# Kernel optimization log

Hardware: AMD Instinct MI355X
Metric: run time of the kernel (lower is better)

## Reference

```python
import jax, jax.numpy as jnp
import numpy as np

B, N, IN_DIM, D, H, E, L = 4, 1024, 128, 512, 8, 4, 3
HD = D // H
LN_EPS = 1e-5


def setup_inputs() -> dict:
    key = jax.random.key(0)
    ks = jax.random.split(key, 16)
    s = lambda fan_in: 1.0 / np.sqrt(fan_in)
    inp = {
        'x': jax.random.normal(ks[0], (B, N, IN_DIM), dtype=jnp.float32),
        'edges': jax.random.normal(ks[1], (B, N, N, E), dtype=jnp.float32),
        'in_w': jax.random.normal(ks[2], (IN_DIM, D), dtype=jnp.float32) * s(IN_DIM),
        'in_b': jnp.zeros((D,), dtype=jnp.float32),
        'qw': jax.random.normal(ks[3], (L, D, D), dtype=jnp.float32) * s(D),
        'qb': jnp.zeros((L, D), dtype=jnp.float32),
        'kw': jax.random.normal(ks[4], (L, D, D), dtype=jnp.float32) * s(D),
        'kb': jnp.zeros((L, D), dtype=jnp.float32),
        'vw': jax.random.normal(ks[5], (L, D, D), dtype=jnp.float32) * s(D),
        'vb': jnp.zeros((L, D), dtype=jnp.float32),
        'ow': jax.random.normal(ks[6], (L, D, D), dtype=jnp.float32) * s(D),
        'ob': jnp.zeros((L, D), dtype=jnp.float32),
        'ew': jax.random.normal(ks[7], (L, E, H), dtype=jnp.float32) * s(E),
        'eb': jnp.zeros((L, H), dtype=jnp.float32),
        'ln_g': jnp.ones((D,), dtype=jnp.float32),
        'ln_b': jnp.zeros((D,), dtype=jnp.float32),
    }
    return inp


def _gat_layer(h, edges, qw, qb, kw, kb, vw, vb, ow, ob, ew, eb):
    # h: (B, N, D); edges: (B, N, N, E)
    q = (h @ qw + qb).reshape(B, N, H, HD)
    k = (h @ kw + kb).reshape(B, N, H, HD)
    v = (h @ vw + vb).reshape(B, N, H, HD)
    logits = jnp.einsum('bihd,bjhd->bhij', q, k) / np.sqrt(HD).astype(np.float32)
    bias = jnp.einsum('bije,eh->bhij', edges, ew) + eb[None, :, None, None]
    attn = jax.nn.softmax(logits + bias, axis=-1)  # (B, H, N, N)
    out = jnp.einsum('bhij,bjhd->bihd', attn, v).reshape(B, N, D)
    return out @ ow + ob


def reference(x, edges, in_w, in_b, qw, qb, kw, kb, vw, vb, ow, ob, ew, eb, ln_g, ln_b):
    h = x @ in_w + in_b  # (B, N, D)
    for l in range(L):
        h = h + _gat_layer(h, edges, qw[l], qb[l], kw[l], kb[l], vw[l], vb[l],
                           ow[l], ob[l], ew[l], eb[l])
    mu = jnp.mean(h, axis=-1, keepdims=True)
    var = jnp.mean(jnp.square(h - mu), axis=-1, keepdims=True)
    return (h - mu) * jax.lax.rsqrt(var + LN_EPS) * ln_g + ln_b
```

## Files before the change

kernel.cpp:

```cpp
#include <hip/hip_runtime.h>
#include <hip/hip_bf16.h>
#include <cstdint>
#include <cstddef>

#define BB 4
#define NN 1024
#define INDIM 128
#define DD 512
#define HH 8
#define EE 4
#define LL 3
#define HDIM 64

typedef __bf16 bf16x8 __attribute__((ext_vector_type(8)));
typedef _Float16 f16x8 __attribute__((ext_vector_type(8)));
typedef _Float16 h2 __attribute__((ext_vector_type(2)));
typedef float f32x4 __attribute__((ext_vector_type(4)));
typedef unsigned int u32x4 __attribute__((ext_vector_type(4)));

__device__ __forceinline__ unsigned short f2b(float f) {
    union { float f; unsigned int u; } v; v.f = f;
    unsigned int u = v.u;
    unsigned int r = (u + 0x7FFFu + ((u >> 16) & 1u)) >> 16;
    return (unsigned short)r;
}
__device__ __forceinline__ float b2f(unsigned int us) {
    union { unsigned int u; float f; } v; v.u = us << 16; return v.f;
}
__device__ __forceinline__ unsigned short h_bits(_Float16 h) {
    union { _Float16 h; unsigned short u; } v; v.h = h; return v.u;
}
__device__ __forceinline__ h2 u2h2(unsigned int u) {
    union { unsigned int u; h2 h; } v; v.u = u; return v.h;
}
__device__ __forceinline__ unsigned int pkrtz_u32(float a, float b) {
    auto h = __builtin_amdgcn_cvt_pkrtz(a, b);
    union { decltype(h) h; unsigned int u; } v; v.h = h; return v.u;
}

__device__ __forceinline__ void gl_lds16(const unsigned short* g, unsigned short* l) {
    __builtin_amdgcn_global_load_lds(
        (const __attribute__((address_space(1))) void*)g,
        (__attribute__((address_space(3))) void*)l, 16, 0, 0);
}

__device__ __forceinline__ void transpose_tile_body(const float* __restrict__ src,
                                                    unsigned short* __restrict__ dst,
                                                    int K, int Nc) {
    __shared__ float tl[32][33];
    const int n0 = blockIdx.x * 32, k0 = blockIdx.y * 32;
    const int tx = threadIdx.x, ty = threadIdx.y;
#pragma unroll
    for (int r = 0; r < 4; r++) {
        int k = ty + r * 8;
        tl[k][tx] = src[(size_t)(k0 + k) * Nc + n0 + tx];
    }
    __syncthreads();
#pragma unroll
    for (int r = 0; r < 4; r++) {
        int n = ty + r * 8;
        dst[(size_t)(n0 + n) * K + k0 + tx] = f2b(tl[tx][n]);
    }
}

__global__ void k_transpose_in(const float* __restrict__ w, unsigned short* __restrict__ dst) {
    transpose_tile_body(w, dst, INDIM, DD);
}

__global__ void k_transpose_qkvo(const float* __restrict__ qw, const float* __restrict__ kw,
                                 const float* __restrict__ vw, const float* __restrict__ ow,
                                 unsigned short* __restrict__ dst) {
    int zz = blockIdx.z;
    int l = zz >> 2, tsel = zz & 3;
    const float* src = (tsel == 0) ? qw : (tsel == 1) ? kw : (tsel == 2) ? vw : ow;
    src += (size_t)l * DD * DD;
    transpose_tile_body(src, dst + (size_t)zz * DD * DD, DD, DD);
}

__global__ void k_convert(const float* __restrict__ src, unsigned short* __restrict__ dst,
                          long long n4) {
    long long stride = (long long)gridDim.x * blockDim.x;
    for (long long i = blockIdx.x * (long long)blockDim.x + threadIdx.x; i < n4; i += stride) {
        float4 v = reinterpret_cast<const float4*>(src)[i];
        uint2 o;
        o.x = (unsigned)f2b(v.x) | ((unsigned)f2b(v.y) << 16);
        o.y = (unsigned)f2b(v.z) | ((unsigned)f2b(v.w) << 16);
        reinterpret_cast<uint2*>(dst)[i] = o;
    }
}

__global__ __launch_bounds__(256) void k_convert_e2(const float* __restrict__ src,
                                                    unsigned short* __restrict__ dst) {
    __shared__ unsigned short tl[4096];
    const int tile = blockIdx.x;
    const int jb = tile & 15;
    const int it = (tile >> 4) & 63;
    const int b  = tile >> 10;
    const int tid = threadIdx.x;
    const int f4 = tid & 63;
    const int r0 = tid >> 6;
    const int jt = f4 >> 4, w16 = f4 & 15;
    const int lh = w16 >> 2, rr = w16 & 3;
    const int c = jt * 2 + (rr >> 1), q = rr & 1;
#pragma unroll
    for (int rd = 0; rd < 4; rd++) {
        const int lm = rd * 4 + r0;
        const float4 e = *reinterpret_cast<const float4*>(
            &src[(((size_t)b * NN + it * 16 + lm) * NN + jb * 64 + f4) * EE]);
        uint2 o;
        o.x = pkrtz_u32(e.x, e.y);
        o.y = pkrtz_u32(e.z, e.w);
        const int slot = c * 128 + (lh * 16 + lm) * 2 + q;
        *reinterpret_cast<uint2*>(&tl[slot * 4]) = o;
    }
    __syncthreads();
    u32x4* g = reinterpret_cast<u32x4*>(dst) + (size_t)tile * 512;
    const u32x4* s = reinterpret_cast<const u32x4*>(tl);
    __builtin_nontemporal_store(s[tid], g + tid);
    __builtin_nontemporal_store(s[tid + 256], g + tid + 256);
}

__global__ __launch_bounds__(256) void k_gemm(
    const unsigned short* __restrict__ A,
    const unsigned short* __restrict__ Wt0, size_t wstride,
    const float* __restrict__ bias0, const float* __restrict__ bias1, const float* __restrict__ bias2,
    unsigned short* __restrict__ outb, size_t ostride,
    unsigned short* __restrict__ vt_out,
    const unsigned short* __restrict__ residb,
    int Kd)
{
    __shared__ __align__(16) unsigned short As[128 * 32];
    __shared__ __align__(16) unsigned short Bs[64 * 32];
    const int tid = threadIdx.x;
    const int lane = tid & 63, wv = tid >> 6;
    const int wr = wv >> 1, wc = wv & 1;
    const int lm = lane & 15, lh = lane >> 4;
    const int m0 = blockIdx.y * 128, n0 = blockIdx.x * 64;
    const int z = blockIdx.z;
    const unsigned short* Wt = Wt0 + (size_t)z * wstride;
    const float* bias = (z == 0) ? bias0 : (z == 1) ? bias1 : bias2;

    f32x4 acc[4][2] = {};

    const int o0 = tid * 16;
    const int rowA = o0 >> 6, colA = (o0 & 63) >> 1;
    for (int k0 = 0; k0 < Kd; k0 += 32) {
        __syncthreads();
        gl_lds16(A  + (size_t)(m0 + rowA) * Kd + k0 + colA, As + (o0 >> 1));
        gl_lds16(A  + (size_t)(m0 + 64 + rowA) * Kd + k0 + colA, As + 2048 + (o0 >> 1));
        gl_lds16(Wt + (size_t)(n0 + rowA) * Kd + k0 + colA, Bs + (o0 >> 1));
        __syncthreads();

        bf16x8 af[4], bfg[2];
#pragma unroll
        for (int mi = 0; mi < 4; mi++)
            af[mi] = *reinterpret_cast<const bf16x8*>(&As[(wr * 64 + mi * 16 + lm) * 32 + lh * 8]);
#pragma unroll
        for (int nj = 0; nj < 2; nj++)
            bfg[nj] = *reinterpret_cast<const bf16x8*>(&Bs[(wc * 32 + nj * 16 + lm) * 32 + lh * 8]);
        __builtin_amdgcn_s_setprio(1);
#pragma unroll
        for (int mi = 0; mi < 4; mi++)
#pragma unroll
            for (int nj = 0; nj < 2; nj++)
                acc[mi][nj] = __builtin_amdgcn_mfma_f32_16x16x32_bf16(af[mi], bfg[nj], acc[mi][nj], 0, 0, 0);
        __builtin_amdgcn_s_setprio(0);
    }

    if (vt_out && z == 2) {
        const int j = n0 + wc * 32 + lm;
#pragma unroll
        for (int mi = 0; mi < 4; mi++) {
            const int i = m0 + wr * 64 + mi * 16 + lh * 4;
            const int bb = i >> 10, n = i & (NN - 1);
#pragma unroll
            for (int nj = 0; nj < 2; nj++) {
                const int jj = j + nj * 16;
                const int hh = jj >> 6, d = jj & 63;
                union { unsigned short us[4]; uint2 u; } pk;
#pragma unroll
                for (int r = 0; r < 4; r++)
                    pk.us[r] = h_bits((_Float16)(acc[mi][nj][r] + bias[jj]));
                *reinterpret_cast<uint2*>(
                    &vt_out[(((size_t)bb * HH + hh) * HDIM + d) * NN + n]) = pk.u;
            }
        }
        return;
    }

#pragma unroll
    for (int mi = 0; mi < 4; mi++) {
#pragma unroll
        for (int nj = 0; nj < 2; nj++) {
#pragma unroll
            for (int r = 0; r < 4; r++) {
                int i = m0 + wr * 64 + mi * 16 + lh * 4 + r;
                int j = n0 + wc * 32 + nj * 16 + lm;
                float val = acc[mi][nj][r] + bias[j];
                size_t oidx = (size_t)i * DD + j;
                if (residb) val += b2f(residb[oidx]);
                outb[(size_t)z * ostride + oidx] = f2b(val);
            }
        }
    }
}

template <int JS>
__global__ __launch_bounds__(512) void k_attn_g2(
    const unsigned short* __restrict__ qb,
    const unsigned short* __restrict__ kb,
    const unsigned short* __restrict__ vt,
    const unsigned short* __restrict__ ebt,
    const float* __restrict__ ew,
    const float* __restrict__ ebias,
    int layer,
    unsigned short* __restrict__ outpb,
    float2* __restrict__ mlp)
{
    __shared__ __align__(16) unsigned short e_lds[2][2][4096];
    __shared__ unsigned short p_lds[8][2][16 * 68];
    const int lin = blockIdx.x;
    const int xcd = lin & 7;
    const int s   = lin >> 3;
    const int combo = xcd * 2 + (s >> 5);
    const int itg = s & 31;
    const int b  = combo & 3;
    const int js = combo >> 2;
    const int tid = threadIdx.x;
    const int lane = tid & 63, wv = tid >> 6;
    const int h = wv;
    const int lm = lane & 15, lh = lane >> 4;

    const float LOG2E = 1.44269504f;
    const float ebh = ebias[layer * HH + h] * LOG2E;
    const float qscale = 0.125f * LOG2E;
    h2 w01, w23;
    w01.x = (_Float16)(ew[(layer * EE + 0) * HH + h] * LOG2E);
    w01.y = (_Float16)(ew[(layer * EE + 1) * HH + h] * LOG2E);
    w23.x = (_Float16)(ew[(layer * EE + 2) * HH + h] * LOG2E);
    w23.y = (_Float16)(ew[(layer * EE + 3) * HH + h] * LOG2E);

    bf16x8 aq[2][2];
#pragma unroll
    for (int g = 0; g < 2; g++) {
        const unsigned short* qrow =
            qb + ((size_t)(b * NN) + itg * 32 + g * 16 + lm) * DD + h * HDIM + lh * 8;
        aq[g][0] = *reinterpret_cast<const bf16x8*>(qrow);
        aq[g][1] = *reinterpret_cast<const bf16x8*>(qrow + 32);
    }

    f32x4 acc[2][4] = {};
    float m_run[2] = {-1e30f, -1e30f}, l_run[2] = {0.f, 0.f};

    constexpr int NITER = (NN / JS) / 64;
    const int jlo = js * (NN / JS);
    const int jb0 = jlo >> 6;
    const unsigned short* etile0 = ebt + ((size_t)((b * 64 + itg * 2 + 0) * 16 + jb0)) * 4096;
    const unsigned short* etile1 = ebt + ((size_t)((b * 64 + itg * 2 + 1) * 16 + jb0)) * 4096;
    const unsigned short* kptr = kb + ((size_t)(b * NN) + jlo + lm) * DD + h * HDIM + lh * 8;
    const unsigned short* vptr = vt + (((size_t)(b * HH) + h) * HDIM + lm) * NN + jlo + lh * 8;

    gl_lds16(etile0 + tid * 8, &e_lds[0][0][tid * 8]);
    gl_lds16(etile1 + tid * 8, &e_lds[0][1][tid * 8]);
    __syncthreads();

#pragma unroll
    for (int i = 0; i < NITER; i++) {
        const int cur = i & 1;
        if (i + 1 < NITER) {
            gl_lds16(etile0 + (size_t)(i + 1) * 4096 + tid * 8, &e_lds[cur ^ 1][0][tid * 8]);
            gl_lds16(etile1 + (size_t)(i + 1) * 4096 + tid * 8, &e_lds[cur ^ 1][1][tid * 8]);
        }

        bf16x8 kf[8];
        f16x8  vf[8];
#pragma unroll
        for (int jt = 0; jt < 4; jt++) {
            const unsigned short* kr = kptr + (size_t)i * 64 * DD + (size_t)jt * 16 * DD;
            kf[jt * 2]     = *reinterpret_cast<const bf16x8*>(kr);
            kf[jt * 2 + 1] = *reinterpret_cast<const bf16x8*>(kr + 32);
        }
#pragma unroll
        for (int kc = 0; kc < 2; kc++)
#pragma unroll
            for (int dt = 0; dt < 4; dt++)
                vf[kc * 4 + dt] = *reinterpret_cast<const f16x8*>(
                    vptr + (size_t)dt * 16 * NN + i * 64 + kc * 32);

#pragma unroll
        for (int g = 0; g < 2; g++) {
            f32x4 sreg[4];
#pragma unroll
            for (int jt = 0; jt < 4; jt++) {
                f32x4 t = {};
                t = __builtin_amdgcn_mfma_f32_16x16x32_bf16(kf[jt * 2], aq[g][0], t, 0, 0, 0);
                t = __builtin_amdgcn_mfma_f32_16x16x32_bf16(kf[jt * 2 + 1], aq[g][1], t, 0, 0, 0);
                sreg[jt] = t;
            }

            float pv[16];
#pragma unroll
            for (int c = 0; c < 8; c++) {
                const uint4 ee = *reinterpret_cast<const uint4*>(
                    &e_lds[cur][g][(c * 64 + lane) * 8]);
                const int jt = c >> 1, r0 = (c & 1) * 2;
                pv[jt * 4 + r0] = fmaf(sreg[jt][r0], qscale,
                    __builtin_amdgcn_fdot2(u2h2(ee.x), w01,
                        __builtin_amdgcn_fdot2(u2h2(ee.y), w23, ebh, false), false));
                pv[jt * 4 + r0 + 1] = fmaf(sreg[jt][r0 + 1], qscale,
                    __builtin_amdgcn_fdot2(u2h2(ee.z), w01,
                        __builtin_amdgcn_fdot2(u2h2(ee.w), w23, ebh, false), false));
            }

            float mt = pv[0];
#pragma unroll
            for (int q = 1; q < 16; q++) mt = fmaxf(mt, pv[q]);
            mt = fmaxf(mt, __shfl_xor(mt, 16));
            mt = fmaxf(mt, __shfl_xor(mt, 32));
            float mn = fmaxf(m_run[g], mt);
            float corr = __builtin_amdgcn_exp2f(m_run[g] - mn);
            m_run[g] = mn;
            float ls = 0.f;
#pragma unroll
            for (int q = 0; q < 16; q++) {
                pv[q] = __builtin_amdgcn_exp2f(pv[q] - mn);
                ls += pv[q];
            }
            ls += __shfl_xor(ls, 16);
            ls += __shfl_xor(ls, 32);
            l_run[g] = l_run[g] * corr + ls;

#pragma unroll
            for (int jt = 0; jt < 4; jt++) {
                uint2 u;
                u.x = pkrtz_u32(pv[jt * 4 + 0], pv[jt * 4 + 1]);
                u.y = pkrtz_u32(pv[jt * 4 + 2], pv[jt * 4 + 3]);
                *reinterpret_cast<uint2*>(&p_lds[wv][g][lm * 68 + jt * 16 + lh * 4]) = u;
            }
#pragma unroll
            for (int dt = 0; dt < 4; dt++)
#pragma unroll
                for (int r = 0; r < 4; r++) acc[g][dt][r] *= corr;

#pragma unroll
            for (int kc = 0; kc < 2; kc++) {
                f16x8 pb = *reinterpret_cast<const f16x8*>(
                    &p_lds[wv][g][lm * 68 + kc * 32 + lh * 8]);
#pragma unroll
                for (int dt = 0; dt < 4; dt++)
                    acc[g][dt] = __builtin_amdgcn_mfma_f32_16x16x32_f16(
                        vf[kc * 4 + dt], pb, acc[g][dt], 0, 0, 0);
            }
        }

        __syncthreads();
    }

#pragma unroll
    for (int g = 0; g < 2; g++) {
        const int irow = itg * 32 + g * 16 + lm;
#pragma unroll
        for (int dt = 0; dt < 4; dt++) {
            union { unsigned short us[4]; uint2 u; } pk;
#pragma unroll
            for (int r = 0; r < 4; r++) pk.us[r] = f2b(acc[g][dt][r]);
            *reinterpret_cast<uint2*>(
                &outpb[((size_t)(js * BB + b) * NN + irow) * DD + h * HDIM + dt * 16 + lh * 4]) = pk.u;
        }
        if (lh == 0)
            mlp[((size_t)(js * BB + b) * HH + h) * NN + irow] = make_float2(m_run[g], l_run[g]);
    }
}

template <int JS>
__global__ __launch_bounds__(256) void k_attnred(
    const unsigned short* __restrict__ outpb, const float2* __restrict__ mlp,
    unsigned short* __restrict__ attnob)
{
    const int tid = blockIdx.x * 256 + threadIdx.x;
    const int dc = tid & 7;
    const int h = (tid >> 3) & 7;
    const int n = (tid >> 6) & (NN - 1);
    const int b = tid >> 16;
    float ms[JS], lsv[JS];
    float mstar = -1e30f;
#pragma unroll
    for (int s2 = 0; s2 < JS; s2++) {
        float2 ml = mlp[((size_t)(s2 * BB + b) * HH + h) * NN + n];
        ms[s2] = ml.x; lsv[s2] = ml.y;
        mstar = fmaxf(mstar, ml.x);
    }
    float lstar = 0.f;
    float o[8] = {0.f, 0.f, 0.f, 0.f, 0.f, 0.f, 0.f, 0.f};
#pragma unroll
    for (int s2 = 0; s2 < JS; s2++) {
        float w = __builtin_amdgcn_exp2f(ms[s2] - mstar);
        lstar += w * lsv[s2];
        uint4 a = *reinterpret_cast<const uint4*>(
            &outpb[((size_t)(s2 * BB + b) * NN + n) * DD + h * HDIM + dc * 8]);
        o[0] += w * b2f(a.x & 0xffffu); o[1] += w * b2f(a.x >> 16);
        o[2] += w * b2f(a.y & 0xffffu); o[3] += w * b2f(a.y >> 16);
        o[4] += w * b2f(a.z & 0xffffu); o[5] += w * b2f(a.z >> 16);
        o[6] += w * b2f(a.w & 0xffffu); o[7] += w * b2f(a.w >> 16);
    }
    const float inv = 1.f / lstar;
    union { unsigned short us[8]; uint4 u; } pk;
#pragma unroll
    for (int q = 0; q < 8; q++) pk.us[q] = f2b(o[q] * inv);
    *reinterpret_cast<uint4*>(&attnob[((size_t)b * NN + n) * DD + h * HDIM + dc * 8]) = pk.u;
}

__global__ __launch_bounds__(256) void k_ln(const unsigned short* __restrict__ hb,
                                            const float* __restrict__ g,
                                            const float* __restrict__ bta,
                                            float* __restrict__ out) {
    const int row = blockIdx.x * 4 + (threadIdx.x >> 6);
    const int lane = threadIdx.x & 63;
    const unsigned short* hr = hb + (size_t)row * DD + lane * 8;
    uint4 v = *reinterpret_cast<const uint4*>(hr);
    float vals[8] = { b2f(v.x & 0xffffu), b2f(v.x >> 16), b2f(v.y & 0xffffu), b2f(v.y >> 16),
                      b2f(v.z & 0xffffu), b2f(v.z >> 16), b2f(v.w & 0xffffu), b2f(v.w >> 16) };
    float sum = 0.f, sq = 0.f;
#pragma unroll
    for (int q = 0; q < 8; q++) { sum += vals[q]; sq += vals[q] * vals[q]; }
#pragma unroll
    for (int m = 1; m <= 32; m <<= 1) {
        sum += __shfl_xor(sum, m);
        sq += __shfl_xor(sq, m);
    }
    float mu = sum * (1.f / DD);
    float var = sq * (1.f / DD) - mu * mu;
    float rs = rsqrtf(var + 1e-5f);
    const float* gp = g + lane * 8;
    const float* bp = bta + lane * 8;
    float* op = out + (size_t)row * DD + lane * 8;
#pragma unroll
    for (int q = 0; q < 8; q++) op[q] = (vals[q] - mu) * rs * gp[q] + bp[q];
}

extern "C" void kernel_launch(void* const* d_in, const int* in_sizes, int n_in,
                              void* d_out, int out_size, void* d_ws, size_t ws_size,
                              hipStream_t stream) {
    (void)in_sizes; (void)n_in; (void)out_size; (void)ws_size;
    const float* x     = (const float*)d_in[0];
    const float* edges = (const float*)d_in[1];
    const float* in_w  = (const float*)d_in[2];
    const float* in_b  = (const float*)d_in[3];
    const float* qw    = (const float*)d_in[4];
    const float* qbias = (const float*)d_in[5];
    const float* kw    = (const float*)d_in[6];
    const float* kbias = (const float*)d_in[7];
    const float* vw    = (const float*)d_in[8];
    const float* vbias = (const float*)d_in[9];
    const float* ow    = (const float*)d_in[10];
    const float* obias = (const float*)d_in[11];
    const float* ew    = (const float*)d_in[12];
    const float* ebias = (const float*)d_in[13];
    const float* ln_g  = (const float*)d_in[14];
    const float* ln_b  = (const float*)d_in[15];
    float* out = (float*)d_out;

    constexpr int JS = 4;
    char* ws = (char*)d_ws;
    size_t off = 0;
    auto alloc = [&](size_t bytes) -> void* {
        void* p = ws + off;
        off += (bytes + 255) & ~(size_t)255;
        return p;
    };
    const size_t M = (size_t)BB * NN;
    unsigned short* hb    = (unsigned short*)alloc(M * DD * 2);
    unsigned short* xb    = (unsigned short*)alloc(M * INDIM * 2);
    unsigned short* wt_in = (unsigned short*)alloc((size_t)DD * INDIM * 2);
    unsigned short* wt    = (unsigned short*)alloc((size_t)12 * DD * DD * 2);
    unsigned short* qkvb  = (unsigned short*)alloc((size_t)3 * M * DD * 2);
    unsigned short* vtb   = (unsigned short*)alloc(M * DD * 2);
    unsigned short* attnob= (unsigned short*)alloc(M * DD * 2);
    const size_t edgeElems = (size_t)BB * NN * NN * EE;
    unsigned short* ebt   = (unsigned short*)alloc(edgeElems * 2);
    unsigned short* outpb = (unsigned short*)alloc((size_t)JS * M * DD * 2);
    float2*         mlp   = (float2*)        alloc((size_t)JS * BB * HH * NN * 8);
    const size_t BND = M * DD;

    k_transpose_in<<<dim3(DD / 32, INDIM / 32), dim3(32, 8), 0, stream>>>(in_w, wt_in);
    k_transpose_qkvo<<<dim3(DD / 32, DD / 32, 12), dim3(32, 8), 0, stream>>>(qw, kw, vw, ow, wt);
    k_convert<<<dim3(512), dim3(256), 0, stream>>>(x, xb, (long long)(M * INDIM / 4));
    k_convert_e2<<<dim3(4096), dim3(256), 0, stream>>>(edges, ebt);

    k_gemm<<<dim3(8, 32, 1), dim3(256), 0, stream>>>(
        xb, wt_in, (size_t)0, in_b, in_b, in_b, hb, (size_t)0,
        (unsigned short*)nullptr, (const unsigned short*)nullptr, INDIM);

    for (int l = 0; l < LL; l++) {
        k_gemm<<<dim3(8, 32, 3), dim3(256), 0, stream>>>(
            hb, wt + (size_t)(l * 4) * DD * DD, (size_t)DD * DD,
            qbias + l * DD, kbias + l * DD, vbias + l * DD,
            qkvb, BND, vtb, (const unsigned short*)nullptr, DD);

        k_attn_g2<JS><<<dim3(512), dim3(512), 0, stream>>>(
            qkvb, qkvb + BND, vtb, ebt, ew, ebias, l, outpb, mlp);
        k_attnred<JS><<<dim3((unsigned)(M * HH * 8 / 256)), dim3(256), 0, stream>>>(
            outpb, mlp, attnob);

        k_gemm<<<dim3(8, 32, 1), dim3(256), 0, stream>>>(
            attnob, wt + (size_t)(l * 4 + 3) * DD * DD, (size_t)0,
            obias + l * DD, obias + l * DD, obias + l * DD,
            hb, (size_t)0, (unsigned short*)nullptr, hb, DD);
    }

    k_ln<<<dim3((unsigned)(M / 4)), dim3(256), 0, stream>>>(hb, ln_g, ln_b, out);
}
```

Before: 290.7 us.

## Fuse split-softmax reduction into output projection GEMM prologue

Removes the separate attention-reduction kernel and folds the combination of the JS partial attention outputs, using the running max and sum values, into the A-tile load of the output-projection GEMM. This drops one kernel launch per layer and the write and re-read of the intermediate attention-output buffer. In exchange, each GEMM block now reads JS partial tiles per K step, recomputes the reduction weights for every column block (eight times redundantly), and converts through registers into LDS instead of loading A asynchronously.

Result: slower. 326.0 us (+12.1%).

```diff
diff --git a/kernel.cpp b/kernel.cpp
--- a/kernel.cpp
+++ b/kernel.cpp
@@ -200,6 +200,148 @@
                 size_t oidx = (size_t)i * DD + j;
                 if (residb) val += b2f(residb[oidx]);
                 outb[(size_t)z * ostride + oidx] = f2b(val);
+            }
+        }
+    }
+}
+
+template <int JS>
+__global__ __launch_bounds__(256) void k_gemm_red(
+    const unsigned short* __restrict__ outpb,
+    const float2* __restrict__ mlp,
+    const unsigned short* __restrict__ Wt,
+    const float* __restrict__ bias,
+    unsigned short* __restrict__ outb,
+    const unsigned short* __restrict__ residb)
+{
+    __shared__ __align__(16) unsigned short As[128 * 32];
+    __shared__ __align__(16) unsigned short Bs[64 * 32];
+    const int tid = threadIdx.x;
+    const int lane = tid & 63, wv = tid >> 6;
+    const int wr = wv >> 1, wc = wv & 1;
+    const int lm = lane & 15, lh = lane >> 4;
+    const int m0 = blockIdx.y * 128, n0 = blockIdx.x * 64;
+    const size_t BND = (size_t)BB * NN * DD;
+
+    f32x4 acc[4][2] = {};
+
+    const int o0 = tid * 16;
+    const int rowA = o0 >> 6, colA = (o0 & 63) >> 1;
+    const int i_lo = m0 + rowA, i_hi = m0 + 64 + rowA;
+    const int bidx = m0 >> 10;
+    const int n_lo = i_lo & (NN - 1), n_hi = i_hi & (NN - 1);
+
+#pragma unroll
+    for (int h8 = 0; h8 < 8; h8++) {
+        float w_lo[JS], w_hi[JS];
+        {
+            float msv[JS], lsv[JS], mstar = -1e30f;
+#pragma unroll
+            for (int s = 0; s < JS; s++) {
+                float2 ml = mlp[((size_t)(s * BB + bidx) * HH + h8) * NN + n_lo];
+                msv[s] = ml.x; lsv[s] = ml.y; mstar = fmaxf(mstar, ml.x);
+            }
+            float lstar = 0.f;
+#pragma unroll
+            for (int s = 0; s < JS; s++) {
+                w_lo[s] = __builtin_amdgcn_exp2f(msv[s] - mstar);
+                lstar += w_lo[s] * lsv[s];
+            }
+            const float inv = 1.f / lstar;
+#pragma unroll
+            for (int s = 0; s < JS; s++) w_lo[s] *= inv;
+        }
+        {
+            float msv[JS], lsv[JS], mstar = -1e30f;
+#pragma unroll
+            for (int s = 0; s < JS; s++) {
+                float2 ml = mlp[((size_t)(s * BB + bidx) * HH + h8) * NN + n_hi];
+                msv[s] = ml.x; lsv[s] = ml.y; mstar = fmaxf(mstar, ml.x);
+            }
+            float lstar = 0.f;
+#pragma unroll
+            for (int s = 0; s < JS; s++) {
+                w_hi[s] = __builtin_amdgcn_exp2f(msv[s] - mstar);
+                lstar += w_hi[s] * lsv[s];
+            }
+            const float inv = 1.f / lstar;
+#pragma unroll
+            for (int s = 0; s < JS; s++) w_hi[s] *= inv;
+        }
+
+#pragma unroll
+        for (int kk = 0; kk < 2; kk++) {
+            const int k0 = h8 * 64 + kk * 32;
+
+            uint4 alo[JS], ahi[JS];
+#pragma unroll
+            for (int s = 0; s < JS; s++) {
+                alo[s] = *reinterpret_cast<const uint4*>(
+                    &outpb[(size_t)s * BND + (size_t)i_lo * DD + k0 + colA]);
+                ahi[s] = *reinterpret_cast<const uint4*>(
+                    &outpb[(size_t)s * BND + (size_t)i_hi * DD + k0 + colA]);
+            }
+            union { unsigned short us[8]; uint4 u; } plo, phi;
+            {
+                float o[8] = {0,0,0,0,0,0,0,0};
+#pragma unroll
+                for (int s = 0; s < JS; s++) {
+                    o[0] += w_lo[s] * b2f(alo[s].x & 0xffffu); o[1] += w_lo[s] * b2f(alo[s].x >> 16);
+                    o[2] += w_lo[s] * b2f(alo[s].y & 0xffffu); o[3] += w_lo[s] * b2f(alo[s].y >> 16);
+                    o[4] += w_lo[s] * b2f(alo[s].z & 0xffffu); o[5] += w_lo[s] * b2f(alo[s].z >> 16);
+                    o[6] += w_lo[s] * b2f(alo[s].w & 0xffffu); o[7] += w_lo[s] * b2f(alo[s].w >> 16);
+                }
+#pragma unroll
+                for (int q = 0; q < 8; q++) plo.us[q] = f2b(o[q]);
+            }
+            {
+                float o[8] = {0,0,0,0,0,0,0,0};
+#pragma unroll
+                for (int s = 0; s < JS; s++) {
+                    o[0] += w_hi[s] * b2f(ahi[s].x & 0xffffu); o[1] += w_hi[s] * b2f(ahi[s].x >> 16);
+                    o[2] += w_hi[s] * b2f(ahi[s].y & 0xffffu); o[3] += w_hi[s] * b2f(ahi[s].y >> 16);
+                    o[4] += w_hi[s] * b2f(ahi[s].z & 0xffffu); o[5] += w_hi[s] * b2f(ahi[s].z >> 16);
+                    o[6] += w_hi[s] * b2f(ahi[s].w & 0xffffu); o[7] += w_hi[s] * b2f(ahi[s].w >> 16);
+                }
+#pragma unroll
+                for (int q = 0; q < 8; q++) phi.us[q] = f2b(o[q]);
+            }
+
+            __syncthreads();
+            *reinterpret_cast<uint4*>(&As[o0 >> 1]) = plo.u;
+            *reinterpret_cast<uint4*>(&As[2048 + (o0 >> 1)]) = phi.u;
+            gl_lds16(Wt + (size_t)(n0 + rowA) * DD + k0 + colA, Bs + (o0 >> 1));
+            __syncthreads();
+
+            bf16x8 af[4], bfg[2];
+#pragma unroll
+            for (int mi = 0; mi < 4; mi++)
+                af[mi] = *reinterpret_cast<const bf16x8*>(&As[(wr * 64 + mi * 16 + lm) * 32 + lh * 8]);
+#pragma unroll
+            for (int nj = 0; nj < 2; nj++)
+                bfg[nj] = *reinterpret_cast<const bf16x8*>(&Bs[(wc * 32 + nj * 16 + lm) * 32 + lh * 8]);
+            __builtin_amdgcn_s_setprio(1);
+#pragma unroll
+            for (int mi = 0; mi < 4; mi++)
+#pragma unroll
+                for (int nj = 0; nj < 2; nj++)
+                    acc[mi][nj] = __builtin_amdgcn_mfma_f32_16x16x32_bf16(af[mi], bfg[nj], acc[mi][nj], 0, 0, 0);
+            __builtin_amdgcn_s_setprio(0);
+        }
+    }
+
+#pragma unroll
+    for (int mi = 0; mi < 4; mi++) {
+#pragma unroll
+        for (int nj = 0; nj < 2; nj++) {
+#pragma unroll
+            for (int r = 0; r < 4; r++) {
+                int i = m0 + wr * 64 + mi * 16 + lh * 4 + r;
+                int j = n0 + wc * 32 + nj * 16 + lm;
+                float val = acc[mi][nj][r] + bias[j];
+                size_t oidx = (size_t)i * DD + j;
+                val += b2f(residb[oidx]);
+                outb[oidx] = f2b(val);
             }
         }
     }
@@ -372,44 +514,6 @@
     }
 }
 
-template <int JS>
-__global__ __launch_bounds__(256) void k_attnred(
-    const unsigned short* __restrict__ outpb, const float2* __restrict__ mlp,
-    unsigned short* __restrict__ attnob)
-{
-    const int tid = blockIdx.x * 256 + threadIdx.x;
-    const int dc = tid & 7;
-    const int h = (tid >> 3) & 7;
-    const int n = (tid >> 6) & (NN - 1);
-    const int b = tid >> 16;
-    float ms[JS], lsv[JS];
-    float mstar = -1e30f;
-#pragma unroll
-    for (int s2 = 0; s2 < JS; s2++) {
-        float2 ml = mlp[((size_t)(s2 * BB + b) * HH + h) * NN + n];
-        ms[s2] = ml.x; lsv[s2] = ml.y;
-        mstar = fmaxf(mstar, ml.x);
-    }
-    float lstar = 0.f;
-    float o[8] = {0.f, 0.f, 0.f, 0.f, 0.f, 0.f, 0.f, 0.f};
-#pragma unroll
-    for (int s2 = 0; s2 < JS; s2++) {
-        float w = __builtin_amdgcn_exp2f(ms[s2] - mstar);
-        lstar += w * lsv[s2];
-        uint4 a = *reinterpret_cast<const uint4*>(
-            &outpb[((size_t)(s2 * BB + b) * NN + n) * DD + h * HDIM + dc * 8]);
-        o[0] += w * b2f(a.x & 0xffffu); o[1] += w * b2f(a.x >> 16);
-        o[2] += w * b2f(a.y & 0xffffu); o[3] += w * b2f(a.y >> 16);
-        o[4] += w * b2f(a.z & 0xffffu); o[5] += w * b2f(a.z >> 16);
-        o[6] += w * b2f(a.w & 0xffffu); o[7] += w * b2f(a.w >> 16);
-    }
-    const float inv = 1.f / lstar;
-    union { unsigned short us[8]; uint4 u; } pk;
-#pragma unroll
-    for (int q = 0; q < 8; q++) pk.us[q] = f2b(o[q] * inv);
-    *reinterpret_cast<uint4*>(&attnob[((size_t)b * NN + n) * DD + h * HDIM + dc * 8]) = pk.u;
-}
-
 __global__ __launch_bounds__(256) void k_ln(const unsigned short* __restrict__ hb,
                                             const float* __restrict__ g,
                                             const float* __restrict__ bta,
@@ -475,7 +579,6 @@
     unsigned short* wt    = (unsigned short*)alloc((size_t)12 * DD * DD * 2);
     unsigned short* qkvb  = (unsigned short*)alloc((size_t)3 * M * DD * 2);
     unsigned short* vtb   = (unsigned short*)alloc(M * DD * 2);
-    unsigned short* attnob= (unsigned short*)alloc(M * DD * 2);
     const size_t edgeElems = (size_t)BB * NN * NN * EE;
     unsigned short* ebt   = (unsigned short*)alloc(edgeElems * 2);
     unsigned short* outpb = (unsigned short*)alloc((size_t)JS * M * DD * 2);
@@ -499,13 +602,10 @@
 
         k_attn_g2<JS><<<dim3(512), dim3(512), 0, stream>>>(
             qkvb, qkvb + BND, vtb, ebt, ew, ebias, l, outpb, mlp);
-        k_attnred<JS><<<dim3((unsigned)(M * HH * 8 / 256)), dim3(256), 0, stream>>>(
-            outpb, mlp, attnob);
-
-        k_gemm<<<dim3(8, 32, 1), dim3(256), 0, stream>>>(
-            attnob, wt + (size_t)(l * 4 + 3) * DD * DD, (size_t)0,
-            obias + l * DD, obias + l * DD, obias + l * DD,
-            hb, (size_t)0, (unsigned short*)nullptr, hb, DD);
+
+        k_gemm_red<JS><<<dim3(8, 32, 1), dim3(256), 0, stream>>>(
+            outpb, mlp, wt + (size_t)(l * 4 + 3) * DD * DD,
+            obias + l * DD, hb, hb);
     }
 
     k_ln<<<dim3((unsigned)(M / 4)), dim3(256), 0, stream>>>(hb, ln_g, ln_b, out);
```
